# Kernel tuning notes

Hardware: AMD Instinct MI355X
Metric: run time of the kernel (lower is better)

The kernel has to match this reference:

```python
import jax, jax.numpy as jnp
import numpy as np

B, H, S, DK = 2, 8, 4096, 64


def setup_inputs() -> dict:
    key = jax.random.key(0)
    kq, kk, kv = jax.random.split(key, 3)
    queries = jax.random.normal(kq, (B, H, S, DK), dtype=jnp.float32)
    keys = jax.random.normal(kk, (B, H, S, DK), dtype=jnp.float32)
    values = jax.random.normal(kv, (B, H, S, DK), dtype=jnp.float32)
    # causal mask: 1.0 where attention is disallowed (strictly upper triangle)
    mask = jnp.triu(jnp.ones((S, S), dtype=jnp.float32), k=1)
    return {"queries": queries, "keys": keys, "values": values, "d_k": DK, "mask": mask}


def reference(queries, keys, values, d_k, mask):
    # scores: [B, H, S, S]
    scale = 1.0 / jnp.sqrt(jnp.float32(d_k))
    scores = jnp.einsum("bhqd,bhkd->bhqk", queries, keys) * scale
    if mask is not None:
        scores = scores + (-1e9) * mask  # broadcast [S,S] over [B,H,S,S]
    weights = jax.nn.softmax(scores, axis=-1)
    return jnp.einsum("bhqk,bhkd->bhqd", weights, values)
```

## Files before the change

kernel.cpp:

```cpp
#include <hip/hip_runtime.h>

typedef __bf16 bf16x8 __attribute__((ext_vector_type(8)));
typedef unsigned short u16x8 __attribute__((ext_vector_type(8)));
typedef unsigned short u16x4 __attribute__((ext_vector_type(4)));
typedef float f32x4 __attribute__((ext_vector_type(4)));

#define MFMA16(a, b, c) __builtin_amdgcn_mfma_f32_16x16x32_bf16((a), (b), (c), 0, 0, 0)

constexpr int SEQ  = 4096;
constexpr int DH   = 64;
constexpr int BH   = 16;
constexpr int LSTR = 72;
constexpr float SCALE_LOG2E = 0.125f * 1.44269504088896f;

__device__ __forceinline__ unsigned short f2bf(float f) {
  unsigned int u = __float_as_uint(f);
  u += 0x7fffu + ((u >> 16) & 1u);
  return (unsigned short)(u >> 16);
}

__global__ __launch_bounds__(256)
void prep_9990093930993(const float* __restrict__ K, const float* __restrict__ V,
                        unsigned short* __restrict__ Kb, unsigned short* __restrict__ Vtb) {
  const int tile = blockIdx.x, bh = blockIdx.y, tid = threadIdx.x;

  {
    const int row = tid >> 2;
    const int c0  = (tid & 3) * 16;
    const float* kr = K + (((long)bh * SEQ + tile * 64) + row) * DH + c0;
    float4 x0 = *(const float4*)(kr);
    float4 x1 = *(const float4*)(kr + 4);
    float4 x2 = *(const float4*)(kr + 8);
    float4 x3 = *(const float4*)(kr + 12);
    u16x8 a, b;
    a[0]=f2bf(x0.x); a[1]=f2bf(x0.y); a[2]=f2bf(x0.z); a[3]=f2bf(x0.w);
    a[4]=f2bf(x1.x); a[5]=f2bf(x1.y); a[6]=f2bf(x1.z); a[7]=f2bf(x1.w);
    b[0]=f2bf(x2.x); b[1]=f2bf(x2.y); b[2]=f2bf(x2.z); b[3]=f2bf(x2.w);
    b[4]=f2bf(x3.x); b[5]=f2bf(x3.y); b[6]=f2bf(x3.z); b[7]=f2bf(x3.w);
    unsigned short* ko = Kb + (((long)bh * SEQ + tile * 64) + row) * DH + c0;
    *(u16x8*)ko = a;
    *(u16x8*)(ko + 8) = b;
  }

  {
    const int d  = tid & 63;
    const int kg = tid >> 6;
    const float* vp = V + ((long)bh * SEQ + tile * 64) * DH;
    unsigned short* op = Vtb + (((long)bh * 64 + tile) * 64 + d) * 64 + kg * 16;
    #pragma unroll
    for (int h = 0; h < 2; ++h) {
      u16x8 o;
      #pragma unroll
      for (int j = 0; j < 8; ++j)
        o[j] = f2bf(vp[(kg * 16 + h * 8 + j) * DH + d]);
      *(u16x8*)(op + h * 8) = o;
    }
  }
}

__global__ __launch_bounds__(256, 2)
void attn3_9990093930993(const float* __restrict__ Qg,
                         const unsigned short* __restrict__ Kb,
                         const unsigned short* __restrict__ Vtb,
                         float* __restrict__ Og) {
  __shared__ unsigned short Kt[2][64 * LSTR];
  __shared__ unsigned short Vt[2][64 * LSTR];
  __shared__ unsigned short Pt[4][16 * LSTR];

  const int tid  = threadIdx.x;
  const int wave = tid >> 6;
  const int lane = tid & 63;
  const int l16  = lane & 15;
  const int lg   = lane >> 4;
  const long bh  = blockIdx.y;

  const float*          Qp = Qg  + bh * (long)(SEQ * DH);
  const unsigned short* Kp = Kb  + bh * (long)(SEQ * DH);
  const unsigned short* Vp = Vtb + bh * (long)(SEQ * DH);
  float*                Op = Og  + bh * (long)(SEQ * DH);

  const int srow = tid >> 2;
  const int scol = (tid & 3) * 16;
  const int f    = tid * 16;

  bf16x8 vone;
  {
    u16x8 t1;
    #pragma unroll
    for (int j = 0; j < 8; ++j) t1[j] = 0x3F80;
    vone = __builtin_bit_cast(bf16x8, t1);
  }

  u16x8 pk0, pk1, pv0, pv1;

  #pragma unroll 1
  for (int seg = 0; seg < 2; ++seg) {
    const int qt = seg ? (int)blockIdx.x : 63 - (int)blockIdx.x;
    const int qrow0 = qt * 64 + wave * 16;

    bf16x8 qf[2];
    {
      const float* qr = Qp + (long)(qrow0 + l16) * DH + lg * 8;
      #pragma unroll
      for (int s = 0; s < 2; ++s) {
        float4 a = *(const float4*)(qr + s * 32);
        float4 b = *(const float4*)(qr + s * 32 + 4);
        u16x8 t2;
        t2[0] = f2bf(a.x * SCALE_LOG2E); t2[1] = f2bf(a.y * SCALE_LOG2E);
        t2[2] = f2bf(a.z * SCALE_LOG2E); t2[3] = f2bf(a.w * SCALE_LOG2E);
        t2[4] = f2bf(b.x * SCALE_LOG2E); t2[5] = f2bf(b.y * SCALE_LOG2E);
        t2[6] = f2bf(b.z * SCALE_LOG2E); t2[7] = f2bf(b.w * SCALE_LOG2E);
        qf[s] = __builtin_bit_cast(bf16x8, t2);
      }
    }

    f32x4 oacc[4] = {};
    f32x4 accl   = {};

    pk0 = *(const u16x8*)(Kp + f); pk1 = *(const u16x8*)(Kp + f + 8);
    pv0 = *(const u16x8*)(Vp + f); pv1 = *(const u16x8*)(Vp + f + 8);

    #pragma unroll 1
    for (int t = 0; t <= qt; ++t) {
      const int buf = t & 1;
      *(u16x8*)&Kt[buf][srow * LSTR + scol]     = pk0;
      *(u16x8*)&Kt[buf][srow * LSTR + scol + 8] = pk1;
      *(u16x8*)&Vt[buf][srow * LSTR + scol]     = pv0;
      *(u16x8*)&Vt[buf][srow * LSTR + scol + 8] = pv1;
      __syncthreads();

      if (t < qt) {
        const unsigned short* ks = Kp + (long)(t + 1) * 4096;
        const unsigned short* vs = Vp + (long)(t + 1) * 4096;
        pk0 = *(const u16x8*)(ks + f); pk1 = *(const u16x8*)(ks + f + 8);
        pv0 = *(const u16x8*)(vs + f); pv1 = *(const u16x8*)(vs + f + 8);
      }

      float sv[16];
      #pragma unroll
      for (int kt = 0; kt < 4; ++kt) {
        bf16x8 kf0 = __builtin_bit_cast(bf16x8, *(const u16x8*)&Kt[buf][(kt*16 + l16) * LSTR + lg * 8]);
        bf16x8 kf1 = __builtin_bit_cast(bf16x8, *(const u16x8*)&Kt[buf][(kt*16 + l16) * LSTR + 32 + lg * 8]);
        f32x4 st = {0.f, 0.f, 0.f, 0.f};
        st = MFMA16(qf[0], kf0, st);
        st = MFMA16(qf[1], kf1, st);
        #pragma unroll
        for (int r = 0; r < 4; ++r) sv[kt * 4 + r] = st[r];
      }
      if (t == qt) {
        #pragma unroll
        for (int kt = 0; kt < 4; ++kt) {
          const int kg = t * 64 + kt * 16 + l16;
          #pragma unroll
          for (int r = 0; r < 4; ++r) {
            const int qg = qrow0 + lg * 4 + r;
            if (kg > qg) sv[kt * 4 + r] = -1e30f;
          }
        }
      }

      #pragma unroll
      for (int kt = 0; kt < 4; ++kt) {
        #pragma unroll
        for (int r = 0; r < 4; ++r) {
          const float p = __builtin_amdgcn_exp2f(sv[kt * 4 + r]);
          Pt[wave][(lg * 4 + r) * LSTR + kt * 16 + l16] = f2bf(p);
        }
      }

      #pragma unroll
      for (int ks2 = 0; ks2 < 2; ++ks2) {
        bf16x8 pf = __builtin_bit_cast(bf16x8, *(const u16x8*)&Pt[wave][l16 * LSTR + ks2 * 32 + lg * 8]);
        accl = MFMA16(pf, vone, accl);
        #pragma unroll
        for (int dt = 0; dt < 4; ++dt) {
          bf16x8 vf = __builtin_bit_cast(bf16x8, *(const u16x8*)&Vt[buf][(dt*16 + l16) * LSTR + ks2 * 32 + lg * 8]);
          oacc[dt] = MFMA16(pf, vf, oacc[dt]);
        }
      }
    }

    #pragma unroll
    for (int r = 0; r < 4; ++r) {
      const float inv = 1.0f / accl[r];
      float* orow = Op + (long)(qrow0 + lg * 4 + r) * DH + l16;
      #pragma unroll
      for (int dt = 0; dt < 4; ++dt)
        orow[dt * 16] = oacc[dt][r] * inv;
    }
    __syncthreads();
  }
}

__global__ __launch_bounds__(256, 2)
void attn_fwd_fb_9990093930993(const float* __restrict__ Qg, const float* __restrict__ Kg,
                               const float* __restrict__ Vg, float* __restrict__ Og) {
  constexpr int FSTR = 88;
  __shared__ unsigned short Kt[64 * FSTR];
  __shared__ unsigned short Vt[64 * FSTR];
  __shared__ unsigned short Pt[4][16 * FSTR];
  const int tid = threadIdx.x, wave = tid >> 6, lane = tid & 63;
  const int l16 = lane & 15, lg = lane >> 4;
  const int qtile = blockIdx.x; const long bh = blockIdx.y;
  const float* Qp = Qg + bh * (long)(SEQ * DH);
  const float* Kp = Kg + bh * (long)(SEQ * DH);
  const float* Vp = Vg + bh * (long)(SEQ * DH);
  float* Op = Og + bh * (long)(SEQ * DH);
  const int qrow0 = qtile * 64 + wave * 16;
  bf16x8 qf[2];
  {
    const float* qr = Qp + (long)(qrow0 + l16) * DH + lg * 8;
    #pragma unroll
    for (int s = 0; s < 2; ++s) {
      float4 a = *(const float4*)(qr + s * 32);
      float4 b = *(const float4*)(qr + s * 32 + 4);
      u16x8 t2;
      t2[0]=f2bf(a.x*0.125f); t2[1]=f2bf(a.y*0.125f); t2[2]=f2bf(a.z*0.125f); t2[3]=f2bf(a.w*0.125f);
      t2[4]=f2bf(b.x*0.125f); t2[5]=f2bf(b.y*0.125f); t2[6]=f2bf(b.z*0.125f); t2[7]=f2bf(b.w*0.125f);
      qf[s] = __builtin_bit_cast(bf16x8, t2);
    }
  }
  float m[4] = {-1e30f,-1e30f,-1e30f,-1e30f}, lsum[4] = {0,0,0,0};
  f32x4 oacc[4] = {};
  for (int t = 0; t <= qtile; ++t) {
    const int kvb = t * 64;
    #pragma unroll
    for (int j = 0; j < 4; ++j) {
      const int idx = j * 256 + tid, row = idx >> 4, c4 = (idx & 15) * 4;
      const long goff = (long)(kvb + row) * DH + c4;
      float4 kx = *(const float4*)(Kp + goff);
      float4 vx = *(const float4*)(Vp + goff);
      u16x4 kb; kb[0]=f2bf(kx.x); kb[1]=f2bf(kx.y); kb[2]=f2bf(kx.z); kb[3]=f2bf(kx.w);
      *(u16x4*)&Kt[row * FSTR + c4] = kb;
      Vt[(c4+0)*FSTR+row]=f2bf(vx.x); Vt[(c4+1)*FSTR+row]=f2bf(vx.y);
      Vt[(c4+2)*FSTR+row]=f2bf(vx.z); Vt[(c4+3)*FSTR+row]=f2bf(vx.w);
    }
    __syncthreads();
    float sv[16];
    #pragma unroll
    for (int kt = 0; kt < 4; ++kt) {
      bf16x8 kf0 = __builtin_bit_cast(bf16x8, *(const u16x8*)&Kt[(kt*16+l16)*FSTR + lg*8]);
      bf16x8 kf1 = __builtin_bit_cast(bf16x8, *(const u16x8*)&Kt[(kt*16+l16)*FSTR + 32 + lg*8]);
      f32x4 st = {0,0,0,0};
      st = MFMA16(qf[0], kf0, st); st = MFMA16(qf[1], kf1, st);
      const int kg = kvb + kt*16 + l16;
      #pragma unroll
      for (int r = 0; r < 4; ++r) {
        const int qg = qrow0 + lg*4 + r;
        sv[kt*4+r] = (kg > qg) ? -1e30f : st[r];
      }
    }
    float alpha[4], psum[4];
    #pragma unroll
    for (int r = 0; r < 4; ++r) {
      float rm = fmaxf(fmaxf(sv[r], sv[4+r]), fmaxf(sv[8+r], sv[12+r]));
      #pragma unroll
      for (int d = 1; d < 16; d <<= 1) rm = fmaxf(rm, __shfl_xor(rm, d));
      const float mn = fmaxf(m[r], rm);
      alpha[r] = __expf(m[r] - mn); m[r] = mn; psum[r] = 0.f;
    }
    #pragma unroll
    for (int kt = 0; kt < 4; ++kt)
      #pragma unroll
      for (int r = 0; r < 4; ++r) {
        const float p = __expf(sv[kt*4+r] - m[r]);
        psum[r] += p;
        Pt[wave][(lg*4+r)*FSTR + kt*16 + l16] = f2bf(p);
      }
    #pragma unroll
    for (int r = 0; r < 4; ++r) {
      float ps = psum[r];
      #pragma unroll
      for (int d = 1; d < 16; d <<= 1) ps += __shfl_xor(ps, d);
      lsum[r] = lsum[r] * alpha[r] + ps;
    }
    #pragma unroll
    for (int dt = 0; dt < 4; ++dt)
      #pragma unroll
      for (int r = 0; r < 4; ++r) oacc[dt][r] *= alpha[r];
    #pragma unroll
    for (int ks2 = 0; ks2 < 2; ++ks2) {
      bf16x8 pf = __builtin_bit_cast(bf16x8, *(const u16x8*)&Pt[wave][l16*FSTR + ks2*32 + lg*8]);
      #pragma unroll
      for (int dt = 0; dt < 4; ++dt) {
        bf16x8 vf = __builtin_bit_cast(bf16x8, *(const u16x8*)&Vt[(dt*16+l16)*FSTR + ks2*32 + lg*8]);
        oacc[dt] = MFMA16(pf, vf, oacc[dt]);
      }
    }
    __syncthreads();
  }
  #pragma unroll
  for (int r = 0; r < 4; ++r) {
    const float inv = 1.0f / lsum[r];
    float* orow = Op + (long)(qrow0 + lg*4 + r) * DH + l16;
    #pragma unroll
    for (int dt = 0; dt < 4; ++dt) orow[dt*16] = oacc[dt][r] * inv;
  }
}

extern "C" void kernel_launch(void* const* d_in, const int* in_sizes, int n_in,
                              void* d_out, int out_size, void* d_ws, size_t ws_size,
                              hipStream_t stream) {
  (void)in_sizes; (void)n_in; (void)out_size;
  const float* Q = (const float*)d_in[0];
  const float* K = (const float*)d_in[1];
  const float* V = (const float*)d_in[2];
  float* O = (float*)d_out;

  const size_t TSZ = (size_t)BH * SEQ * DH * sizeof(unsigned short);
  if (ws_size >= 2 * TSZ) {
    unsigned short* Kb  = (unsigned short*)d_ws;
    unsigned short* Vtb = Kb + (size_t)BH * SEQ * DH;
    prep_9990093930993<<<dim3(SEQ / 64, BH), dim3(256), 0, stream>>>(K, V, Kb, Vtb);
    attn3_9990093930993<<<dim3(SEQ / 128, BH), dim3(256), 0, stream>>>(Q, Kb, Vtb, O);
  } else {
    attn_fwd_fb_9990093930993<<<dim3(SEQ / 64, BH), dim3(256), 0, stream>>>(Q, K, V, O);
  }
}
```

Baseline: 201.8 us.

## Rebalance causal work scheduling and transpose QK MFMA for vectorized P stores

Replaces the fixed two-segment pairing grid (512 blocks of paired q-tiles) with a 768-block 1D schedule. Long q-tiles for half the heads run as single-segment blocks first, then paired short/long segments, then the remaining long tiles. This is meant to reduce tail imbalance and raise occupancy, with the launch-bounds minimum blocks raised from 2 to 3. It also swaps the MFMA operand order so each lane holds four consecutive keys of one query row. That lets the P tile be written to LDS as one 4-element vector store instead of four scalar stores. The higher occupancy target may force register spilling.

Result: no change. 199.2 us (-1.3%).

```diff
diff --git a/kernel.cpp b/kernel.cpp
--- a/kernel.cpp
+++ b/kernel.cpp
@@ -58,8 +58,8 @@
   }
 }
 
-__global__ __launch_bounds__(256, 2)
-void attn3_9990093930993(const float* __restrict__ Qg,
+__global__ __launch_bounds__(256, 3)
+void attn4_9990093930993(const float* __restrict__ Qg,
                          const unsigned short* __restrict__ Kb,
                          const unsigned short* __restrict__ Vtb,
                          float* __restrict__ Og) {
@@ -72,7 +72,16 @@
   const int lane = tid & 63;
   const int l16  = lane & 15;
   const int lg   = lane >> 4;
-  const long bh  = blockIdx.y;
+
+  int nseg, qt0, qt1 = 0, bhi;
+  {
+    const int id = blockIdx.x;
+    if (id < 256)      { nseg = 1; qt0 = 63 - (id >> 3); bhi = id & 7; }
+    else if (id < 512) { const int j = id - 256; nseg = 2; const int p = j >> 4;
+                         qt0 = 31 - p; qt1 = p; bhi = j & 15; }
+    else               { const int j = id - 512; nseg = 1; qt0 = 32 + (j >> 3); bhi = 8 + (j & 7); }
+  }
+  const long bh = bhi;
 
   const float*          Qp = Qg  + bh * (long)(SEQ * DH);
   const unsigned short* Kp = Kb  + bh * (long)(SEQ * DH);
@@ -94,8 +103,8 @@
   u16x8 pk0, pk1, pv0, pv1;
 
   #pragma unroll 1
-  for (int seg = 0; seg < 2; ++seg) {
-    const int qt = seg ? (int)blockIdx.x : 63 - (int)blockIdx.x;
+  for (int seg = 0; seg < nseg; ++seg) {
+    const int qt = (seg == 0) ? qt0 : qt1;
     const int qrow0 = qt * 64 + wave * 16;
 
     bf16x8 qf[2];
@@ -115,7 +124,7 @@
     }
 
     f32x4 oacc[4] = {};
-    f32x4 accl   = {};
+    f32x4 accl    = {};
 
     pk0 = *(const u16x8*)(Kp + f); pk1 = *(const u16x8*)(Kp + f + 8);
     pv0 = *(const u16x8*)(Vp + f); pv1 = *(const u16x8*)(Vp + f + 8);
@@ -142,30 +151,30 @@
         bf16x8 kf0 = __builtin_bit_cast(bf16x8, *(const u16x8*)&Kt[buf][(kt*16 + l16) * LSTR + lg * 8]);
         bf16x8 kf1 = __builtin_bit_cast(bf16x8, *(const u16x8*)&Kt[buf][(kt*16 + l16) * LSTR + 32 + lg * 8]);
         f32x4 st = {0.f, 0.f, 0.f, 0.f};
-        st = MFMA16(qf[0], kf0, st);
-        st = MFMA16(qf[1], kf1, st);
+        st = MFMA16(kf0, qf[0], st);
+        st = MFMA16(kf1, qf[1], st);
         #pragma unroll
         for (int r = 0; r < 4; ++r) sv[kt * 4 + r] = st[r];
       }
       if (t == qt) {
+        const int qg = qrow0 + l16;
         #pragma unroll
         for (int kt = 0; kt < 4; ++kt) {
-          const int kg = t * 64 + kt * 16 + l16;
+          const int k0 = t * 64 + kt * 16 + lg * 4;
           #pragma unroll
-          for (int r = 0; r < 4; ++r) {
-            const int qg = qrow0 + lg * 4 + r;
-            if (kg > qg) sv[kt * 4 + r] = -1e30f;
-          }
+          for (int r = 0; r < 4; ++r)
+            if (k0 + r > qg) sv[kt * 4 + r] = -1e30f;
         }
       }
 
       #pragma unroll
       for (int kt = 0; kt < 4; ++kt) {
-        #pragma unroll
-        for (int r = 0; r < 4; ++r) {
-          const float p = __builtin_amdgcn_exp2f(sv[kt * 4 + r]);
-          Pt[wave][(lg * 4 + r) * LSTR + kt * 16 + l16] = f2bf(p);
-        }
+        u16x4 w;
+        w[0] = f2bf(__builtin_amdgcn_exp2f(sv[kt * 4 + 0]));
+        w[1] = f2bf(__builtin_amdgcn_exp2f(sv[kt * 4 + 1]));
+        w[2] = f2bf(__builtin_amdgcn_exp2f(sv[kt * 4 + 2]));
+        w[3] = f2bf(__builtin_amdgcn_exp2f(sv[kt * 4 + 3]));
+        *(u16x4*)&Pt[wave][l16 * LSTR + kt * 16 + lg * 4] = w;
       }
 
       #pragma unroll
@@ -312,7 +321,7 @@
     unsigned short* Kb  = (unsigned short*)d_ws;
     unsigned short* Vtb = Kb + (size_t)BH * SEQ * DH;
     prep_9990093930993<<<dim3(SEQ / 64, BH), dim3(256), 0, stream>>>(K, V, Kb, Vtb);
-    attn3_9990093930993<<<dim3(SEQ / 128, BH), dim3(256), 0, stream>>>(Q, Kb, Vtb, O);
+    attn4_9990093930993<<<dim3(768), dim3(256), 0, stream>>>(Q, Kb, Vtb, O);
   } else {
     attn_fwd_fb_9990093930993<<<dim3(SEQ / 64, BH), dim3(256), 0, stream>>>(Q, K, V, O);
   }
```
